# Performance work log

Measured on AMD Instinct MI355X. Metric: run time of the kernel, lower is better.

Reference implementation:

```python
import jax, jax.numpy as jnp
import numpy as np

B, T, C, H, FF, BOT = 2, 2048, 1024, 16, 4096, 64
D = C // H
EPS = 1e-5

def _ln(x, g, b):
    m = jnp.mean(x, axis=-1, keepdims=True)
    v = jnp.mean(jnp.square(x - m), axis=-1, keepdims=True)
    return (x - m) * jax.lax.rsqrt(v + EPS) * g + b

def setup_inputs() -> dict:
    key = jax.random.key(0)
    ks = jax.random.split(key, 20)
    def lin(k, fan_in, shape):
        return jax.random.normal(k, shape, jnp.float32) * (1.0 / np.sqrt(fan_in))
    inp = {
        "x": jax.random.normal(ks[0], (B, T, C), jnp.float32),
        # causal mask: masked_fill where mask == 0
        "attn_mask": jnp.tril(jnp.ones((T, T), jnp.int32))[None, None, :, :],
        "Wq": lin(ks[1], C, (C, C)), "bq": jnp.zeros((C,), jnp.float32),
        "Wk": lin(ks[2], C, (C, C)), "bk": jnp.zeros((C,), jnp.float32),
        "Wv": lin(ks[3], C, (C, C)), "bv": jnp.zeros((C,), jnp.float32),
        "Wo": lin(ks[4], C, (C, C)), "bo": jnp.zeros((C,), jnp.float32),
        "g1": jnp.ones((C,), jnp.float32), "beta1": jnp.zeros((C,), jnp.float32),
        "g2": jnp.ones((C,), jnp.float32), "beta2": jnp.zeros((C,), jnp.float32),
        "W1": lin(ks[5], C, (C, FF)), "bf1": jnp.zeros((FF,), jnp.float32),
        "W2": lin(ks[6], FF, (FF, C)), "bf2": jnp.zeros((C,), jnp.float32),
        "Wd": lin(ks[7], C, (C, BOT)), "bd": jnp.zeros((BOT,), jnp.float32),
        "Wu": lin(ks[8], BOT, (BOT, C)), "bu": jnp.zeros((C,), jnp.float32),
    }
    return inp

def reference(x, attn_mask, Wq, bq, Wk, bk, Wv, bv, Wo, bo,
              g1, beta1, g2, beta2, W1, bf1, W2, bf2, Wd, bd, Wu, bu):
    # --- attention sublayer ---
    xn = _ln(x, g1, beta1)
    q = (xn @ Wq + bq).reshape(B, T, H, D)
    k = (xn @ Wk + bk).reshape(B, T, H, D)
    v = (xn @ Wv + bv).reshape(B, T, H, D)
    scores = jnp.einsum('bthd,bshd->bhts', q, k) / jnp.sqrt(jnp.float32(D))
    scores = jnp.where(attn_mask == 0, -jnp.inf, scores)
    w = jax.nn.softmax(scores, axis=-1)
    attn = jnp.einsum('bhts,bshd->bthd', w, v).reshape(B, T, C)
    x = x + attn @ Wo + bo
    # --- FFN + adapter sublayer ---
    xn2 = _ln(x, g2, beta2)
    h = jax.nn.relu(xn2 @ W1 + bf1) @ W2 + bf2
    h = h + jax.nn.relu(h @ Wd + bd) @ Wu + bu  # adapter residual
    return x + h
```

## Files before the change

kernel.cpp:

```cpp
#include <hip/hip_runtime.h>
#include <cstdint>
#include <cstddef>

typedef unsigned short u16;
typedef __attribute__((ext_vector_type(4))) short short4v;
typedef __attribute__((ext_vector_type(8))) short short8;
typedef __attribute__((ext_vector_type(4))) float f32x4;

__device__ __forceinline__ float bf2f(u16 h) { return __uint_as_float(((unsigned)h) << 16); }
__device__ __forceinline__ u16 f2bf(float f) {
    unsigned u = __float_as_uint(f);
    unsigned r = (u + 0x7fffu + ((u >> 16) & 1u)) >> 16;
    return (u16)r;
}
__device__ __forceinline__ u16 f2bf_fast(float f) {
    return (u16)((__float_as_uint(f) + 0x8000u) >> 16);
}

__device__ __forceinline__ void gl_lds16(const void* g, void* l) {
    __builtin_amdgcn_global_load_lds((const __attribute__((address_space(1))) void*)g,
                                     (__attribute__((address_space(3))) void*)l, 16, 0, 0);
}

__global__ __launch_bounds__(256) void detect_kernel(const unsigned* __restrict__ x,
                                                     int* __restrict__ flag) {
    __shared__ int cnt[256];
    int c = 0;
    for (int i = threadIdx.x; i < 4096; i += 256) {
        unsigned lo = x[i] & 0xFFFFu;
        unsigned e = (lo >> 7) & 0xFFu;
        c += (e >= 100u && e <= 150u) ? 1 : 0;
    }
    cnt[threadIdx.x] = c;
    __syncthreads();
    for (int s = 128; s > 0; s >>= 1) {
        if (threadIdx.x < s) cnt[threadIdx.x] += cnt[threadIdx.x + s];
        __syncthreads();
    }
    if (threadIdx.x == 0) *flag = (cnt[0] > 2048) ? 1 : 0;
}

struct ParamCvt {
    const void* src[12];
    int off[12];
    int n[12];
};
__global__ __launch_bounds__(256) void param_cvt_kernel(ParamCvt pc, float* __restrict__ dst,
                                                        const int* __restrict__ flag) {
    const int bf = *flag;
    const int s = blockIdx.x;
    const void* sp = pc.src[s];
    float* dp = dst + pc.off[s];
    const int n = pc.n[s];
    for (int i = threadIdx.x; i < n; i += 256)
        dp[i] = bf ? bf2f(((const u16*)sp)[i]) : ((const float*)sp)[i];
}

__global__ __launch_bounds__(256) void cvt_x_kernel(const void* __restrict__ x,
                                                    u16* __restrict__ xb,
                                                    const int* __restrict__ flag) {
    const int bf = *flag;
    const int i0 = (blockIdx.x * 256 + threadIdx.x) * 4;
    u16 o[4];
    if (bf) {
        *(uint2*)o = *(const uint2*)((const u16*)x + i0);
    } else {
        float4 f = *(const float4*)((const float*)x + i0);
        o[0] = f2bf(f.x); o[1] = f2bf(f.y); o[2] = f2bf(f.z); o[3] = f2bf(f.w);
    }
    *(uint2*)&xb[i0] = *(uint2*)o;
}

struct TAll {
    const void* src[8];
    u16* dst[8];
    int R[8], C[8];
    int off[8];
};
__global__ __launch_bounds__(256) void transpose_all_kernel(TAll t,
                                                            const int* __restrict__ flag) {
    const int bf = *flag;
    __shared__ u16 tile[32][33];
    int bid = blockIdx.x;
    int m = 0;
#pragma unroll
    for (int i = 1; i < 8; i++) m = (bid >= t.off[i]) ? i : m;
    int local = bid - t.off[m];
    const int R = t.R[m], C = t.C[m];
    const int tilesx = C >> 5;
    const int bx = local % tilesx, by = local / tilesx;
    const void* src = t.src[m];
    u16* dst = t.dst[m];
    const int tx = threadIdx.x & 31, ty = threadIdx.x >> 5;
#pragma unroll
    for (int i = 0; i < 32; i += 8) {
        size_t idx = (size_t)(by * 32 + ty + i) * C + bx * 32 + tx;
        tile[ty + i][tx] = bf ? ((const u16*)src)[idx] : f2bf(((const float*)src)[idx]);
    }
    __syncthreads();
#pragma unroll
    for (int i = 0; i < 32; i += 8)
        dst[(size_t)(bx * 32 + ty + i) * R + by * 32 + tx] = tile[tx][ty + i];
}

__global__ __launch_bounds__(256) void ln_kernel(const u16* __restrict__ X,
                                                 const float* __restrict__ G,
                                                 const float* __restrict__ Be,
                                                 u16* __restrict__ Y) {
    const int row = blockIdx.x;
    const int tid = threadIdx.x;
    const int lane = tid & 63, wave = tid >> 6;
    const u16* xr = X + (size_t)row * 1024;
    u16 vbuf[4];
    *(uint2*)vbuf = *(const uint2*)&xr[tid * 4];
    float f[4];
    float s = 0.f, sq = 0.f;
#pragma unroll
    for (int j = 0; j < 4; j++) { f[j] = bf2f(vbuf[j]); s += f[j]; sq += f[j] * f[j]; }
#pragma unroll
    for (int m = 1; m < 64; m <<= 1) { s += __shfl_xor(s, m, 64); sq += __shfl_xor(sq, m, 64); }
    __shared__ float rs_[4], rq_[4];
    if (lane == 0) { rs_[wave] = s; rq_[wave] = sq; }
    __syncthreads();
    float S = rs_[0] + rs_[1] + rs_[2] + rs_[3];
    float Q2 = rq_[0] + rq_[1] + rq_[2] + rq_[3];
    float mean = S * (1.f / 1024.f);
    float var = Q2 * (1.f / 1024.f) - mean * mean;
    float rstd = rsqrtf(var + 1e-5f);
    u16 o[4];
#pragma unroll
    for (int j = 0; j < 4; j++) {
        int c2 = tid * 4 + j;
        float y = (f[j] - mean) * rstd * G[c2] + Be[c2];
        o[j] = f2bf(y);
    }
    *(uint2*)&Y[(size_t)row * 1024 + tid * 4] = *(uint2*)o;
}

template <int TAG>
__global__ __launch_bounds__(256) void gemm_bt_kernel(const u16* __restrict__ A,
                                                      const u16* __restrict__ Bt,
                                                      const float* __restrict__ bias,
                                                      const u16* __restrict__ res1,
                                                      const u16* __restrict__ res2,
                                                      void* __restrict__ out,
                                                      void* __restrict__ out_k,
                                                      void* __restrict__ out_v,
                                                      int M, int N, int K, int relu, int mode,
                                                      const int* __restrict__ flag) {
    __shared__ __align__(16) u16 As[2][128 * 32];
    __shared__ __align__(16) u16 Bs[2][128 * 32];
    const int tid = threadIdx.x;
    const int wave = tid >> 6, lane = tid & 63;
    const int m0 = blockIdx.y * 128, n0 = blockIdx.x * 128;
    const int wm = (wave >> 1) * 64, wn = (wave & 1) * 64;

    f32x4 acc[4][4];
#pragma unroll
    for (int i = 0; i < 4; i++)
#pragma unroll
        for (int j = 0; j < 4; j++) acc[i][j] = (f32x4){0.f, 0.f, 0.f, 0.f};

    const int lr4 = lane >> 2;
    const int sc4 = ((lane & 3) ^ ((lane >> 3) & 3));

    const int Ksub = K / (int)gridDim.z;
    const int kbeg = blockIdx.z * Ksub;

    auto stage = [&](int k0, int bufi) {
#pragma unroll
        for (int c = 0; c < 2; c++) {
            int rbase = wave * 32 + c * 16;
            int arow = m0 + rbase + lr4;
            int brow = n0 + rbase + lr4;
            if (brow > N - 1) brow = N - 1;
            gl_lds16(A + (size_t)arow * K + k0 + sc4 * 8, &As[bufi][rbase * 32 + lane * 8]);
            gl_lds16(Bt + (size_t)brow * K + k0 + sc4 * 8, &Bs[bufi][rbase * 32 + lane * 8]);
        }
    };

    stage(kbeg, 0);
    __syncthreads();
    const int nk = Ksub >> 5;
    for (int ik = 0; ik < nk; ik++) {
        const int cur = ik & 1;
        if (ik + 1 < nk) stage(kbeg + ((ik + 1) << 5), cur ^ 1);
        short8 af[4], bf[4];
        const int cc = (lane >> 4) ^ ((lane >> 1) & 3);
#pragma unroll
        for (int i = 0; i < 4; i++)
            af[i] = *(const short8*)&As[cur][(wm + i * 16 + (lane & 15)) * 32 + cc * 8];
#pragma unroll
        for (int j = 0; j < 4; j++)
            bf[j] = *(const short8*)&Bs[cur][(wn + j * 16 + (lane & 15)) * 32 + cc * 8];
#pragma unroll
        for (int i = 0; i < 4; i++)
#pragma unroll
            for (int j = 0; j < 4; j++)
                acc[i][j] = __builtin_amdgcn_mfma_f32_16x16x32_bf16(af[i], bf[j], acc[i][j], 0, 0, 0);
        __syncthreads();
    }

    if (mode == 3) {
        float* po = (float*)out + (size_t)blockIdx.z * M * N;
#pragma unroll
        for (int j = 0; j < 4; j++) {
            int col = n0 + wn + j * 16 + (lane & 15);
            if (col >= N) continue;
#pragma unroll
            for (int i = 0; i < 4; i++)
#pragma unroll
                for (int r = 0; r < 4; r++) {
                    int row = m0 + wm + i * 16 + (lane >> 4) * 4 + r;
                    po[(size_t)row * N + col] = acc[i][j][r];
                }
        }
        return;
    }

    const int f32out = (mode == 1) && (*flag == 0);
#pragma unroll
    for (int j = 0; j < 4; j++) {
        int col = n0 + wn + j * 16 + (lane & 15);
        if (col >= N) continue;
        float bv = bias ? bias[col] : 0.f;
#pragma unroll
        for (int i = 0; i < 4; i++) {
#pragma unroll
            for (int r = 0; r < 4; r++) {
                int row = m0 + wm + i * 16 + (lane >> 4) * 4 + r;
                float v = acc[i][j][r] + bv;
                if (relu) v = fmaxf(v, 0.f);
                size_t idx = (size_t)row * N + col;
                if (res1) v += bf2f(res1[idx]);
                if (res2) v += bf2f(res2[idx]);
                if (f32out) ((float*)out)[idx] = v;
                else ((u16*)out)[idx] = f2bf(v);
            }
        }
    }
}

template <int TAG>
__global__ __launch_bounds__(512, 4) void gemm128_kernel(const u16* __restrict__ A,
                                                         const u16* __restrict__ Bt,
                                                         const float* __restrict__ bias,
                                                         const u16* __restrict__ res1,
                                                         const u16* __restrict__ res2,
                                                         void* __restrict__ out,
                                                         void* __restrict__ out_k,
                                                         void* __restrict__ out_v,
                                                         int M, int N, int K, int relu, int mode,
                                                         const int* __restrict__ flag) {
    (void)flag; (void)M;
    __shared__ __align__(16) u16 As[2][2][128 * 32];
    __shared__ __align__(16) u16 Bs[2][2][128 * 32];
    const int tid = threadIdx.x;
    const int wave = tid >> 6, lane = tid & 63;
    const int l15 = lane & 15, quad = lane >> 4;
    const int wr = wave & 3, wc = wave >> 2;
    const int m0 = blockIdx.y * 128, n0 = blockIdx.x * 128;
    const int nt = K >> 6;

    const int rsub = lane >> 2;
    const int logc = (lane & 3) ^ ((rsub >> 1) & 3);

    auto stage_pair = [&](int t, int kh) {
        const int buf = t & 1;
        const int kk = (t << 6) + (kh << 5) + logc * 8;
        const int roff = wave * 16 + rsub;
        gl_lds16(A + (size_t)(m0 + roff) * K + kk, &As[buf][kh][wave * 512 + lane * 8]);
        gl_lds16(Bt + (size_t)(n0 + roff) * K + kk, &Bs[buf][kh][wave * 512 + lane * 8]);
    };

    f32x4 acc[2][4];
#pragma unroll
    for (int i = 0; i < 2; i++)
#pragma unroll
        for (int j = 0; j < 4; j++) acc[i][j] = (f32x4){0.f, 0.f, 0.f, 0.f};

    stage_pair(0, 0);
    stage_pair(0, 1);
    stage_pair(1, 0);
    asm volatile("s_waitcnt vmcnt(4)" ::: "memory");
    __builtin_amdgcn_s_barrier();

    const int rx = (l15 >> 1) & 3;
    for (int t = 0; t < nt; t++) {
        const int b = t & 1;
#pragma unroll
        for (int ph = 0; ph < 2; ph++) {
            const int kh = ph;
            short8 af[2], bfr[4];
#pragma unroll
            for (int i = 0; i < 2; i++)
                af[i] = *(const short8*)&As[b][kh][(wr * 32 + i * 16 + l15) * 32 +
                                                   ((quad ^ rx) << 3)];
#pragma unroll
            for (int j = 0; j < 4; j++)
                bfr[j] = *(const short8*)&Bs[b][kh][(wc * 64 + j * 16 + l15) * 32 +
                                                    ((quad ^ rx) << 3)];
            if (ph == 0) { if (t + 1 < nt) stage_pair(t + 1, 1); }
            else         { if (t + 2 < nt) stage_pair(t + 2, 0); }
            __builtin_amdgcn_s_barrier();
            asm volatile("s_waitcnt lgkmcnt(0)" ::: "memory");
            __builtin_amdgcn_s_setprio(1);
#pragma unroll
            for (int i = 0; i < 2; i++)
#pragma unroll
                for (int j = 0; j < 4; j++)
                    acc[i][j] = __builtin_amdgcn_mfma_f32_16x16x32_bf16(
                        af[i], bfr[j], acc[i][j], 0, 0, 0);
            __builtin_amdgcn_s_setprio(0);
            if (ph == 0) {
                if (t + 1 < nt) { asm volatile("s_waitcnt vmcnt(4)" ::: "memory"); }
                else            { asm volatile("s_waitcnt vmcnt(0)" ::: "memory"); }
            } else {
                if (t + 2 < nt)      { asm volatile("s_waitcnt vmcnt(4)" ::: "memory"); }
                else if (t + 1 < nt) { asm volatile("s_waitcnt vmcnt(2)" ::: "memory"); }
            }
            __builtin_amdgcn_s_barrier();
        }
    }

    if (mode == 2) {
        const int region = n0 >> 10;
        if (region < 2) {
            u16* o = (u16*)(region == 0 ? out : out_k);
#pragma unroll
            for (int j = 0; j < 4; j++) {
                const int col = n0 + wc * 64 + j * 16 + l15;
                const float bv = bias[col];
                const int cl = col & 1023;
#pragma unroll
                for (int i = 0; i < 2; i++) {
                    const int row0 = m0 + wr * 32 + i * 16 + quad * 4;
#pragma unroll
                    for (int r = 0; r < 4; r++)
                        o[(size_t)(row0 + r) * 1024 + cl] = f2bf(acc[i][j][r] + bv);
                }
            }
        } else {
            u16* o = (u16*)out_v;
#pragma unroll
            for (int j = 0; j < 4; j++) {
                const int col = n0 + wc * 64 + j * 16 + l15;
                const float bv = bias[col];
                const int cl = col & 1023;
                const int h = cl >> 6, d = cl & 63;
#pragma unroll
                for (int i = 0; i < 2; i++) {
                    const int row_base = m0 + wr * 32 + i * 16 + quad * 4;
                    const int bb = row_base >> 11, tt = row_base & 2047;
                    u16 pk[4];
#pragma unroll
                    for (int r = 0; r < 4; r++) pk[r] = f2bf(acc[i][j][r] + bv);
                    *(uint2*)&o[(((size_t)bb * 16 + h) * 64 + d) * 2048 + tt] = *(uint2*)pk;
                }
            }
        }
        return;
    }
#pragma unroll
    for (int j = 0; j < 4; j++) {
        const int col = n0 + wc * 64 + j * 16 + l15;
        const float bv = bias ? bias[col] : 0.f;
#pragma unroll
        for (int i = 0; i < 2; i++) {
            const int row0 = m0 + wr * 32 + i * 16 + quad * 4;
#pragma unroll
            for (int r = 0; r < 4; r++) {
                float v = acc[i][j][r] + bv;
                if (relu) v = fmaxf(v, 0.f);
                const size_t idx = (size_t)(row0 + r) * N + col;
                if (res1) v += bf2f(res1[idx]);
                if (res2) v += bf2f(res2[idx]);
                ((u16*)out)[idx] = f2bf(v);
            }
        }
    }
}

template <int TAG>
__global__ __launch_bounds__(256) void reduce_kernel(const float* __restrict__ part,
                                                     int nsplit, size_t MN,
                                                     const float* __restrict__ bias, int N,
                                                     const u16* __restrict__ res1,
                                                     const u16* __restrict__ res2,
                                                     void* __restrict__ out,
                                                     int relu, int final_store,
                                                     const int* __restrict__ flag) {
    const size_t i0 = ((size_t)blockIdx.x * 256 + threadIdx.x) * 4;
    float4 s = *(const float4*)&part[i0];
    for (int z = 1; z < nsplit; z++) {
        float4 p = *(const float4*)&part[(size_t)z * MN + i0];
        s.x += p.x; s.y += p.y; s.z += p.z; s.w += p.w;
    }
    const int col = (int)(i0 & (size_t)(N - 1));
    float v[4] = {s.x, s.y, s.z, s.w};
#pragma unroll
    for (int j = 0; j < 4; j++) {
        v[j] += bias[col + j];
        if (relu) v[j] = fmaxf(v[j], 0.f);
    }
    if (res1) {
        u16 r[4]; *(uint2*)r = *(const uint2*)&res1[i0];
#pragma unroll
        for (int j = 0; j < 4; j++) v[j] += bf2f(r[j]);
    }
    if (res2) {
        u16 r[4]; *(uint2*)r = *(const uint2*)&res2[i0];
#pragma unroll
        for (int j = 0; j < 4; j++) v[j] += bf2f(r[j]);
    }
    if (final_store && (*flag == 0)) {
        *(float4*)&((float*)out)[i0] = (float4){v[0], v[1], v[2], v[3]};
    } else {
        u16 o[4];
#pragma unroll
        for (int j = 0; j < 4; j++) o[j] = f2bf(v[j]);
        *(uint2*)&((u16*)out)[i0] = *(uint2*)o;
    }
}

template <int SPLIT>
__global__ __launch_bounds__(256) void flash_kernel(const u16* __restrict__ Q,
                                                    const u16* __restrict__ Kg,
                                                    const u16* __restrict__ VtG,
                                                    u16* __restrict__ O,
                                                    float* __restrict__ pO,
                                                    float* __restrict__ pL) {
    const int tid = threadIdx.x;
    const int wave = tid >> 6, lane = tid & 63;
    int qb, ch;
    if (SPLIT) {
        const int i = blockIdx.x;
        if (i < 32)      { qb = 31 - (i >> 2); ch = i & 3; }
        else if (i < 56) { const int j = i - 32; qb = 23 - j / 3; ch = j % 3; }
        else if (i < 72) { const int j = i - 56; qb = 15 - (j >> 1); ch = j & 1; }
        else             { qb = 7 - (i - 72); ch = 0; }
    } else {
        qb = 31 - blockIdx.x; ch = 0;
    }
    const int bh = blockIdx.y;
    const int t0 = qb * 64;
    const int steps = qb + 1;
    const int ktbeg = SPLIT ? ch * 8 : 0;
    const int ktend = SPLIT ? (steps < ktbeg + 8 ? steps : ktbeg + 8) : steps;
    const size_t base = ((size_t)(bh >> 4) * 2048) * 1024 + (size_t)(bh & 15) * 64;
    const size_t basev = (size_t)bh * 64 * 2048;

    __shared__ __align__(16) u16 Ks[2][64 * 64];
    __shared__ __align__(16) u16 Vt[2][64 * 64];
#if !__has_builtin(__builtin_amdgcn_mfma_f32_16x16x16bf16_1k)
    __shared__ __align__(16) u16 Ps[4][16 * 72];
#endif

    const int l15 = lane & 15, quad = lane >> 4;
    const int rmin = t0 + wave * 16;

    short8 qf[2];
    {
        const u16* qp = Q + base + (size_t)(rmin + l15) * 1024 + quad * 8;
        qf[0] = *(const short8*)qp;
        qf[1] = *(const short8*)(qp + 32);
    }

    const int slr = lane >> 3;
    const int sc8 = (lane & 7) ^ slr;
    const int rb = wave * 16;

    auto stage = [&](int kt, int bufi) {
        gl_lds16(Kg + base + (size_t)(kt * 64 + rb + slr) * 1024 + sc8 * 8,
                 &Ks[bufi][rb * 64 + lane * 8]);
        gl_lds16(Kg + base + (size_t)(kt * 64 + rb + 8 + slr) * 1024 + sc8 * 8,
                 &Ks[bufi][(rb + 8) * 64 + lane * 8]);
        gl_lds16(VtG + basev + (size_t)(rb + slr) * 2048 + kt * 64 + sc8 * 8,
                 &Vt[bufi][rb * 64 + lane * 8]);
        gl_lds16(VtG + basev + (size_t)(rb + 8 + slr) * 2048 + kt * 64 + sc8 * 8,
                 &Vt[bufi][(rb + 8) * 64 + lane * 8]);
    };

    float l_part = 0.f;
    f32x4 oacc[4];
#pragma unroll
    for (int jt = 0; jt < 4; jt++) oacc[jt] = (f32x4){0.f, 0.f, 0.f, 0.f};

    const float Cs = 0.125f * 1.44269504f;

    stage(ktbeg, 0);
    __syncthreads();

    for (int kt = ktbeg; kt < ktend; kt++) {
        const int cur = kt & 1;
        if (kt + 1 < ktend) stage(kt + 1, cur ^ 1);

        short8 kf[2][4];
#pragma unroll
        for (int st = 0; st < 2; st++)
#pragma unroll
            for (int j = 0; j < 4; j++)
                kf[st][j] = *(const short8*)&Ks[cur][(j * 16 + l15) * 64 +
                                                     (((st * 4 + quad) ^ (l15 & 7)) * 8)];
#if __has_builtin(__builtin_amdgcn_mfma_f32_16x16x16bf16_1k)
        short4v vf[4][4];
#pragma unroll
        for (int j = 0; j < 4; j++) {
            int k8 = j * 2 + (quad >> 1);
#pragma unroll
            for (int jt = 0; jt < 4; jt++) {
                int d = jt * 16 + l15;
                vf[j][jt] = *(const short4v*)&Vt[cur][d * 64 + ((k8 ^ (d & 7)) * 8) +
                                                      (quad & 1) * 4];
            }
        }
#else
        short8 vf[2][4];
#pragma unroll
        for (int st = 0; st < 2; st++)
#pragma unroll
            for (int jt = 0; jt < 4; jt++) {
                int d = jt * 16 + l15;
                vf[st][jt] = *(const short8*)&Vt[cur][d * 64 + (((st * 4 + quad) ^ (d & 7)) * 8)];
            }
#endif

        f32x4 s[4];
#pragma unroll
        for (int j = 0; j < 4; j++) s[j] = (f32x4){0.f, 0.f, 0.f, 0.f};
#pragma unroll
        for (int st = 0; st < 2; st++)
#pragma unroll
            for (int j = 0; j < 4; j++)
                s[j] = __builtin_amdgcn_mfma_f32_16x16x32_bf16(kf[st][j], qf[st], s[j], 0, 0, 0);

        const int qrow = rmin + l15;
        const bool needmask = (kt * 64 + 63 > rmin);
        float lp = l_part;
        short4v pj[4];
#pragma unroll
        for (int j = 0; j < 4; j++) {
            union { short4v v; u16 u[4]; } pk;
#pragma unroll
            for (int r = 0; r < 4; r++) {
                float p = __builtin_amdgcn_exp2f(s[j][r] * Cs);
                int key = kt * 64 + j * 16 + quad * 4 + r;
                if (needmask && key > qrow) p = 0.f;
                lp += p;
                pk.u[r] = f2bf_fast(p);
            }
            pj[j] = pk.v;
        }
        l_part = lp;

#if __has_builtin(__builtin_amdgcn_mfma_f32_16x16x16bf16_1k)
#pragma unroll
        for (int jt = 0; jt < 4; jt++)
#pragma unroll
            for (int j = 0; j < 4; j++)
                oacc[jt] = __builtin_amdgcn_mfma_f32_16x16x16bf16_1k(pj[j], vf[j][jt],
                                                                     oacc[jt], 0, 0, 0);
#else
        u16* Pw = Ps[wave];
#pragma unroll
        for (int j = 0; j < 4; j++)
            *(short4v*)&Pw[l15 * 72 + j * 16 + quad * 4] = pj[j];
#pragma unroll
        for (int st = 0; st < 2; st++) {
            short8 pf = *(const short8*)&Pw[l15 * 72 + st * 32 + quad * 8];
#pragma unroll
            for (int jt = 0; jt < 4; jt++)
                oacc[jt] = __builtin_amdgcn_mfma_f32_16x16x32_bf16(pf, vf[st][jt],
                                                                  oacc[jt], 0, 0, 0);
        }
#endif
        __syncthreads();
    }

    float lf = l_part;
    lf += __shfl_xor(lf, 16, 64);
    lf += __shfl_xor(lf, 32, 64);

    if (SPLIT && steps > 8) {
        const size_t ib = ((size_t)bh * 24 + (qb - 8)) * 4 + ch;
        float* po = pO + ib * 4096;
#pragma unroll
        for (int jt = 0; jt < 4; jt++)
#pragma unroll
            for (int r = 0; r < 4; r++)
                po[(wave * 16 + quad * 4 + r) * 64 + jt * 16 + l15] = oacc[jt][r];
        if (quad == 0) pL[ib * 64 + wave * 16 + l15] = lf;
        return;
    }

    {
        float inv[4];
#pragma unroll
        for (int r = 0; r < 4; r++) inv[r] = 1.f / __shfl(lf, quad * 4 + r, 64);
#pragma unroll
        for (int jt = 0; jt < 4; jt++) {
            int d = jt * 16 + l15;
#pragma unroll
            for (int r = 0; r < 4; r++) {
                int t = rmin + quad * 4 + r;
                O[base + (size_t)t * 1024 + d] = f2bf(oacc[jt][r] * inv[r]);
            }
        }
    }
}

__global__ __launch_bounds__(256) void flash_combine_kernel(const float* __restrict__ pO,
                                                            const float* __restrict__ pL,
                                                            u16* __restrict__ O) {
    const int qj = blockIdx.x;
    const int bh = blockIdx.y;
    const int qb = qj + 8;
    const int nch = (qb >> 3) + 1;
    const int tid = threadIdx.x;
    const int row = tid >> 2;
    const int d0 = (tid & 3) * 16;
    const size_t ib = ((size_t)bh * 24 + qj) * 4;

    float acc[16];
#pragma unroll
    for (int k = 0; k < 16; k++) acc[k] = 0.f;
    float lsum = 0.f;
    for (int c = 0; c < nch; c++) {
        const float* po = pO + (ib + c) * 4096 + row * 64 + d0;
#pragma unroll
        for (int v = 0; v < 4; v++) {
            float4 f = *(const float4*)&po[v * 4];
            acc[v * 4 + 0] += f.x; acc[v * 4 + 1] += f.y;
            acc[v * 4 + 2] += f.z; acc[v * 4 + 3] += f.w;
        }
        lsum += pL[(ib + c) * 64 + row];
    }
    const float inv = 1.f / lsum;
    u16 o[16];
#pragma unroll
    for (int k = 0; k < 16; k++) o[k] = f2bf(acc[k] * inv);
    const size_t base = ((size_t)(bh >> 4) * 2048) * 1024 + (size_t)(bh & 15) * 64;
    const int t = qb * 64 + row;
    u16* op = &O[base + (size_t)t * 1024 + d0];
    *(uint4*)op = ((uint4*)o)[0];
    *(uint4*)(op + 8) = ((uint4*)o)[1];
}

extern "C" void kernel_launch(void* const* d_in, const int* in_sizes, int n_in,
                              void* d_out, int out_size, void* d_ws, size_t ws_size,
                              hipStream_t stream) {
    (void)in_sizes; (void)n_in; (void)out_size;
    const void* x   = d_in[0];
    const void* Wq  = d_in[2];  const void* bq  = d_in[3];
    const void* Wk  = d_in[4];  const void* bk  = d_in[5];
    const void* Wv  = d_in[6];  const void* bv  = d_in[7];
    const void* Wo  = d_in[8];  const void* bo  = d_in[9];
    const void* g1  = d_in[10]; const void* be1 = d_in[11];
    const void* g2  = d_in[12]; const void* be2 = d_in[13];
    const void* W1  = d_in[14]; const void* bf1 = d_in[15];
    const void* W2  = d_in[16]; const void* bf2 = d_in[17];
    const void* Wd  = d_in[18]; const void* bd  = d_in[19];
    const void* Wu  = d_in[20]; const void* bu  = d_in[21];

    uint8_t* w8 = (uint8_t*)d_ws;
    int* flag = (int*)w8;
    float* pf = (float*)(w8 + 64);
    u16* wsb = (u16*)(w8 + 64 + 65536);

    const size_t M1 = 1024ull * 1024ull;
    u16* WqT = wsb;
    u16* WkT = wsb + 1 * M1;
    u16* WvT = wsb + 2 * M1;
    u16* WoT = wsb + 3 * M1;
    u16* W1T = wsb + 4 * M1;
    u16* W2T = wsb + 8 * M1;
    u16* WdT = wsb + 12 * M1;
    u16* WuT = wsb + 12 * M1 + 65536;
    u16* S0  = wsb + 12 * M1 + 131072;
    u16* Areg = S0;
    u16* Breg = S0 + 4 * M1;
    u16* ff1  = S0;
    u16* Creg = S0 + 16 * M1;
    u16* Dreg = S0 + 20 * M1;
    u16* Ereg = S0 + 24 * M1;
    u16* xb = Areg;
    u16* xn = Breg; u16* attn = Breg;
    u16* q = Creg;  u16* xn2 = Creg;  u16* bot = Creg;
    u16* kk_ = Dreg; u16* x1 = Dreg;
    u16* VtG = Ereg; u16* hh = Ereg;

    const size_t arena_bytes = (size_t)(64 + 65536) + (40 * M1 + 131072) * 2;
    float* partf = (float*)(w8 + ((arena_bytes + 255) & ~(size_t)255));
    const size_t need = ((arena_bytes + 255) & ~(size_t)255) + 4ull * 4 * M1 * 4;
    const bool sk = ws_size >= need;
    float* flL = partf + 14 * M1;

    float* bqkv_f = pf + 0;
    float* bo_f  = pf + 3072;
    float* bf1_f = pf + 4096;  float* bf2_f = pf + 8192;
    float* bd_f  = pf + 9216;  float* bu_f  = pf + 9280;
    float* g1_f  = pf + 10304; float* be1_f = pf + 11328;
    float* g2_f  = pf + 12352; float* be2_f = pf + 13376;

    detect_kernel<<<1, 256, 0, stream>>>((const unsigned*)x, flag);

    ParamCvt pc;
    const void* srcs[12] = {bq, bk, bv, bo, bf1, bf2, bd, bu, g1, be1, g2, be2};
    int offs[12] = {0, 1024, 2048, 3072, 4096, 8192, 9216, 9280, 10304, 11328, 12352, 13376};
    int ns[12]   = {1024, 1024, 1024, 1024, 4096, 1024, 64, 1024, 1024, 1024, 1024, 1024};
    for (int i = 0; i < 12; i++) { pc.src[i] = srcs[i]; pc.off[i] = offs[i]; pc.n[i] = ns[i]; }
    param_cvt_kernel<<<12, 256, 0, stream>>>(pc, pf, flag);

    cvt_x_kernel<<<4096, 256, 0, stream>>>(x, xb, flag);

    TAll ta;
    const void* tsrc[8] = {Wq, Wk, Wv, Wo, W1, W2, Wd, Wu};
    u16* tdst[8] = {WqT, WkT, WvT, WoT, W1T, W2T, WdT, WuT};
    int tR[8] = {1024, 1024, 1024, 1024, 1024, 4096, 1024, 64};
    int tC[8] = {1024, 1024, 1024, 1024, 4096, 1024, 64, 1024};
    int acc_off = 0;
    for (int i = 0; i < 8; i++) {
        ta.src[i] = tsrc[i]; ta.dst[i] = tdst[i];
        ta.R[i] = tR[i]; ta.C[i] = tC[i];
        ta.off[i] = acc_off;
        acc_off += (tR[i] >> 5) * (tC[i] >> 5);
    }
    transpose_all_kernel<<<acc_off, 256, 0, stream>>>(ta, flag);

    ln_kernel<<<4096, 256, 0, stream>>>(xb, g1_f, be1_f, xn);
    gemm128_kernel<0><<<dim3(24, 32), 512, 0, stream>>>(xn, WqT, bqkv_f, nullptr, nullptr,
                                                        q, kk_, VtG, 4096, 3072, 1024, 0, 2, flag);
    if (sk) {
        flash_kernel<1><<<dim3(80, 32), 256, 0, stream>>>(q, kk_, VtG, attn, partf, flL);
        flash_combine_kernel<<<dim3(24, 32), 256, 0, stream>>>(partf, flL, attn);
    } else {
        flash_kernel<0><<<dim3(32, 32), 256, 0, stream>>>(q, kk_, VtG, attn, nullptr, nullptr);
    }
    gemm128_kernel<1><<<dim3(8, 32), 512, 0, stream>>>(attn, WoT, bo_f, xb, nullptr,
                                                       x1, nullptr, nullptr, 4096, 1024, 1024, 0, 0, flag);
    ln_kernel<<<4096, 256, 0, stream>>>(x1, g2_f, be2_f, xn2);
    gemm128_kernel<2><<<dim3(32, 32), 512, 0, stream>>>(xn2, W1T, bf1_f, nullptr, nullptr,
                                                        ff1, nullptr, nullptr, 4096, 4096, 1024, 1, 0, flag);
    gemm128_kernel<3><<<dim3(8, 32), 512, 0, stream>>>(ff1, W2T, bf2_f, nullptr, nullptr,
                                                       hh, nullptr, nullptr, 4096, 1024, 4096, 0, 0, flag);
    if (sk) {
        gemm_bt_kernel<4><<<dim3(1, 32, 8), 256, 0, stream>>>(hh, WdT, nullptr, nullptr, nullptr,
                                                              partf, nullptr, nullptr, 4096, 64, 1024, 1, 3, flag);
        reduce_kernel<4><<<256, 256, 0, stream>>>(partf, 8, 256 * 1024, bd_f, 64, nullptr, nullptr,
                                                  bot, 1, 0, flag);
    } else {
        gemm_bt_kernel<4><<<dim3(1, 32), 256, 0, stream>>>(hh, WdT, bd_f, nullptr, nullptr,
                                                           bot, nullptr, nullptr, 4096, 64, 1024, 1, 0, flag);
    }
    gemm_bt_kernel<5><<<dim3(8, 32), 256, 0, stream>>>(bot, WuT, bu_f, hh, x1,
                                                       d_out, nullptr, nullptr, 4096, 1024, 64, 0, 1, flag);
}
```

Before: 461.2 us.

## Use 4-wave 128x128 GEMM blocks with larger per-wave tiles and XCD swizzle

Changes the 128x128 GEMM from 8 waves (each computing 32x64) to 4 waves (each computing 64x64), so each thread issues twice as many global-to-LDS loads and holds a 4x4 accumulator array. The aim is more MFMA work per LDS fragment read and less per-wave overhead. It also adds an optional block-index swizzle that spreads neighbouring tiles across the 8 XCDs, enabled for the Wo and W2 GEMMs. The cost is higher register pressure, fewer waves per block to hide latency, and a changed launch-bounds occupancy target.

```diff
diff --git a/kernel.cpp b/kernel.cpp
--- a/kernel.cpp
+++ b/kernel.cpp
@@ -242,7 +242,7 @@
 }
 
 template <int TAG>
-__global__ __launch_bounds__(512, 4) void gemm128_kernel(const u16* __restrict__ A,
+__global__ __launch_bounds__(256, 2) void gemm128_kernel(const u16* __restrict__ A,
                                                          const u16* __restrict__ Bt,
                                                          const float* __restrict__ bias,
                                                          const u16* __restrict__ res1,
@@ -251,6 +251,7 @@
                                                          void* __restrict__ out_k,
                                                          void* __restrict__ out_v,
                                                          int M, int N, int K, int relu, int mode,
+                                                         int swz,
                                                          const int* __restrict__ flag) {
     (void)flag; (void)M;
     __shared__ __align__(16) u16 As[2][2][128 * 32];
@@ -258,8 +259,17 @@
     const int tid = threadIdx.x;
     const int wave = tid >> 6, lane = tid & 63;
     const int l15 = lane & 15, quad = lane >> 4;
-    const int wr = wave & 3, wc = wave >> 2;
-    const int m0 = blockIdx.y * 128, n0 = blockIdx.x * 128;
+    const int wr = wave >> 1, wc = wave & 1;
+    int bx = blockIdx.x, by = blockIdx.y;
+    if (swz) {
+        const int gx = gridDim.x;
+        const int nwg = gx * gridDim.y;
+        const int bid = by * gx + bx;
+        const int sbid = (bid & 7) * (nwg >> 3) + (bid >> 3);
+        bx = sbid % gx;
+        by = sbid / gx;
+    }
+    const int m0 = by * 128, n0 = bx * 128;
     const int nt = K >> 6;
 
     const int rsub = lane >> 2;
@@ -268,21 +278,25 @@
     auto stage_pair = [&](int t, int kh) {
         const int buf = t & 1;
         const int kk = (t << 6) + (kh << 5) + logc * 8;
-        const int roff = wave * 16 + rsub;
-        gl_lds16(A + (size_t)(m0 + roff) * K + kk, &As[buf][kh][wave * 512 + lane * 8]);
-        gl_lds16(Bt + (size_t)(n0 + roff) * K + kk, &Bs[buf][kh][wave * 512 + lane * 8]);
+        const int roff = wave * 32 + rsub;
+        u16* da = &As[buf][kh][wave * 1024 + lane * 8];
+        u16* db = &Bs[buf][kh][wave * 1024 + lane * 8];
+        gl_lds16(A + (size_t)(m0 + roff) * K + kk, da);
+        gl_lds16(A + (size_t)(m0 + roff + 16) * K + kk, da + 512);
+        gl_lds16(Bt + (size_t)(n0 + roff) * K + kk, db);
+        gl_lds16(Bt + (size_t)(n0 + roff + 16) * K + kk, db + 512);
     };
 
-    f32x4 acc[2][4];
-#pragma unroll
-    for (int i = 0; i < 2; i++)
+    f32x4 acc[4][4];
+#pragma unroll
+    for (int i = 0; i < 4; i++)
 #pragma unroll
         for (int j = 0; j < 4; j++) acc[i][j] = (f32x4){0.f, 0.f, 0.f, 0.f};
 
     stage_pair(0, 0);
     stage_pair(0, 1);
     stage_pair(1, 0);
-    asm volatile("s_waitcnt vmcnt(4)" ::: "memory");
+    asm volatile("s_waitcnt vmcnt(8)" ::: "memory");
     __builtin_amdgcn_s_barrier();
 
     const int rx = (l15 >> 1) & 3;
@@ -291,10 +305,10 @@
 #pragma unroll
         for (int ph = 0; ph < 2; ph++) {
             const int kh = ph;
-            short8 af[2], bfr[4];
-#pragma unroll
-            for (int i = 0; i < 2; i++)
-                af[i] = *(const short8*)&As[b][kh][(wr * 32 + i * 16 + l15) * 32 +
+            short8 af[4], bfr[4];
+#pragma unroll
+            for (int i = 0; i < 4; i++)
+                af[i] = *(const short8*)&As[b][kh][(wr * 64 + i * 16 + l15) * 32 +
                                                    ((quad ^ rx) << 3)];
 #pragma unroll
             for (int j = 0; j < 4; j++)
@@ -306,18 +320,18 @@
             asm volatile("s_waitcnt lgkmcnt(0)" ::: "memory");
             __builtin_amdgcn_s_setprio(1);
 #pragma unroll
-            for (int i = 0; i < 2; i++)
+            for (int i = 0; i < 4; i++)
 #pragma unroll
                 for (int j = 0; j < 4; j++)
                     acc[i][j] = __builtin_amdgcn_mfma_f32_16x16x32_bf16(
                         af[i], bfr[j], acc[i][j], 0, 0, 0);
             __builtin_amdgcn_s_setprio(0);
             if (ph == 0) {
-                if (t + 1 < nt) { asm volatile("s_waitcnt vmcnt(4)" ::: "memory"); }
+                if (t + 1 < nt) { asm volatile("s_waitcnt vmcnt(8)" ::: "memory"); }
                 else            { asm volatile("s_waitcnt vmcnt(0)" ::: "memory"); }
             } else {
-                if (t + 2 < nt)      { asm volatile("s_waitcnt vmcnt(4)" ::: "memory"); }
-                else if (t + 1 < nt) { asm volatile("s_waitcnt vmcnt(2)" ::: "memory"); }
+                if (t + 2 < nt)      { asm volatile("s_waitcnt vmcnt(8)" ::: "memory"); }
+                else if (t + 1 < nt) { asm volatile("s_waitcnt vmcnt(4)" ::: "memory"); }
             }
             __builtin_amdgcn_s_barrier();
         }
@@ -333,8 +347,8 @@
                 const float bv = bias[col];
                 const int cl = col & 1023;
 #pragma unroll
-                for (int i = 0; i < 2; i++) {
-                    const int row0 = m0 + wr * 32 + i * 16 + quad * 4;
+                for (int i = 0; i < 4; i++) {
+                    const int row0 = m0 + wr * 64 + i * 16 + quad * 4;
 #pragma unroll
                     for (int r = 0; r < 4; r++)
                         o[(size_t)(row0 + r) * 1024 + cl] = f2bf(acc[i][j][r] + bv);
@@ -349,8 +363,8 @@
                 const int cl = col & 1023;
                 const int h = cl >> 6, d = cl & 63;
 #pragma unroll
-                for (int i = 0; i < 2; i++) {
-                    const int row_base = m0 + wr * 32 + i * 16 + quad * 4;
+                for (int i = 0; i < 4; i++) {
+                    const int row_base = m0 + wr * 64 + i * 16 + quad * 4;
                     const int bb = row_base >> 11, tt = row_base & 2047;
                     u16 pk[4];
 #pragma unroll
@@ -366,8 +380,8 @@
         const int col = n0 + wc * 64 + j * 16 + l15;
         const float bv = bias ? bias[col] : 0.f;
 #pragma unroll
-        for (int i = 0; i < 2; i++) {
-            const int row0 = m0 + wr * 32 + i * 16 + quad * 4;
+        for (int i = 0; i < 4; i++) {
+            const int row0 = m0 + wr * 64 + i * 16 + quad * 4;
 #pragma unroll
             for (int r = 0; r < 4; r++) {
                 float v = acc[i][j][r] + bv;
@@ -728,21 +742,21 @@
     transpose_all_kernel<<<acc_off, 256, 0, stream>>>(ta, flag);
 
     ln_kernel<<<4096, 256, 0, stream>>>(xb, g1_f, be1_f, xn);
-    gemm128_kernel<0><<<dim3(24, 32), 512, 0, stream>>>(xn, WqT, bqkv_f, nullptr, nullptr,
-                                                        q, kk_, VtG, 4096, 3072, 1024, 0, 2, flag);
+    gemm128_kernel<0><<<dim3(24, 32), 256, 0, stream>>>(xn, WqT, bqkv_f, nullptr, nullptr,
+                                                        q, kk_, VtG, 4096, 3072, 1024, 0, 2, 0, flag);
     if (sk) {
         flash_kernel<1><<<dim3(80, 32), 256, 0, stream>>>(q, kk_, VtG, attn, partf, flL);
         flash_combine_kernel<<<dim3(24, 32), 256, 0, stream>>>(partf, flL, attn);
     } else {
         flash_kernel<0><<<dim3(32, 32), 256, 0, stream>>>(q, kk_, VtG, attn, nullptr, nullptr);
     }
-    gemm128_kernel<1><<<dim3(8, 32), 512, 0, stream>>>(attn, WoT, bo_f, xb, nullptr,
-                                                       x1, nullptr, nullptr, 4096, 1024, 1024, 0, 0, flag);
+    gemm128_kernel<1><<<dim3(8, 32), 256, 0, stream>>>(attn, WoT, bo_f, xb, nullptr,
+                                                       x1, nullptr, nullptr, 4096, 1024, 1024, 0, 0, 1, flag);
     ln_kernel<<<4096, 256, 0, stream>>>(x1, g2_f, be2_f, xn2);
-    gemm128_kernel<2><<<dim3(32, 32), 512, 0, stream>>>(xn2, W1T, bf1_f, nullptr, nullptr,
-                                                        ff1, nullptr, nullptr, 4096, 4096, 1024, 1, 0, flag);
-    gemm128_kernel<3><<<dim3(8, 32), 512, 0, stream>>>(ff1, W2T, bf2_f, nullptr, nullptr,
-                                                       hh, nullptr, nullptr, 4096, 1024, 4096, 0, 0, flag);
+    gemm128_kernel<2><<<dim3(32, 32), 256, 0, stream>>>(xn2, W1T, bf1_f, nullptr, nullptr,
+                                                        ff1, nullptr, nullptr, 4096, 4096, 1024, 1, 0, 0, flag);
+    gemm128_kernel<3><<<dim3(8, 32), 256, 0, stream>>>(ff1, W2T, bf2_f, nullptr, nullptr,
+                                                       hh, nullptr, nullptr, 4096, 1024, 4096, 0, 0, 1, flag);
     if (sk) {
         gemm_bt_kernel<4><<<dim3(1, 32, 8), 256, 0, stream>>>(hh, WdT, nullptr, nullptr, nullptr,
                                                               partf, nullptr, nullptr, 4096, 64, 1024, 1, 3, flag);
```

Result: slower. 492.5 us (+6.8%).
